# Performance work log

Measured on AMD Instinct MI355X. Metric: run time of the kernel, lower is better.

## Reference

```python
import jax, jax.numpy as jnp
import numpy as np

NUM_HEADS = 16
ROPE_THETA = 10000.0


def _rope_angles(seq_len, head_dim, dtype):
    # lucidrains rotary_embedding_torch: freqs = theta^(-2i/d) for i in 0..d/2,
    # angles = pos * freq, then each angle repeated twice along last dim (interleaved pairs).
    inv_freq = 1.0 / (ROPE_THETA ** (jnp.arange(0, head_dim, 2, dtype=jnp.float32) / head_dim))
    angles = jnp.arange(seq_len, dtype=jnp.float32)[:, None] * inv_freq  # [N, D/2]
    return jnp.repeat(angles, 2, axis=-1).astype(dtype)  # [N, D]


def _rotate_half(t):
    # interleaved pairs: (x0, x1) -> (-x1, x0)
    t1 = t[..., ::2]
    t2 = t[..., 1::2]
    return jnp.stack([-t2, t1], axis=-1).reshape(t.shape)


def _apply_rope(t, cos, sin):
    # t: [B, H, N, D]; cos/sin: [N, D]
    return t * cos + _rotate_half(t) * sin


def setup_inputs() -> dict:
    key = jax.random.key(0)
    ks = jax.random.split(key, 5)
    B, N, C = 4, 1024, 1024
    return {
        "x": jax.random.normal(ks[0], (B, N, C), dtype=jnp.float32),
        "w_qkv": jax.random.normal(ks[1], (C, 3 * C), dtype=jnp.float32) * (C ** -0.5),
        "b_qkv": jax.random.normal(ks[2], (3 * C,), dtype=jnp.float32) * 0.02,
        "w_proj": jax.random.normal(ks[3], (C, C), dtype=jnp.float32) * (C ** -0.5),
        "b_proj": jax.random.normal(ks[4], (C,), dtype=jnp.float32) * 0.02,
    }


def reference(x, w_qkv, b_qkv, w_proj, b_proj):
    B, N, C = x.shape
    H = NUM_HEADS
    D = C // H

    qkv = x @ w_qkv + b_qkv  # [B, N, 3C]
    qkv = qkv.reshape(B, N, 3, H, D).transpose(2, 0, 3, 1, 4)  # [3, B, H, N, D]
    q, k, v = qkv[0], qkv[1], qkv[2]

    ang = _rope_angles(N, D, x.dtype)
    cos, sin = jnp.cos(ang), jnp.sin(ang)
    q = _apply_rope(q, cos, sin)
    k = _apply_rope(k, cos, sin)

    scale = D ** -0.5  # SDPA default scale
    scores = jnp.einsum("bhqd,bhkd->bhqk", q, k) * scale
    attn = jax.nn.softmax(scores, axis=-1)
    out = jnp.einsum("bhqk,bhkd->bhqd", attn, v)  # [B, H, N, D]

    out = out.transpose(0, 2, 1, 3).reshape(B, N, C)
    return out @ w_proj + b_proj
```

## Files before the change

### kernel.cpp

```cpp
#include <hip/hip_runtime.h>
#include <math.h>

#define BB 4
#define NN 1024
#define CC 1024
#define HH 16
#define DD 64
#define N3 3072

typedef __attribute__((ext_vector_type(8))) short bf16x8;
typedef __attribute__((ext_vector_type(8))) _Float16 f16x8;
typedef __attribute__((ext_vector_type(4))) _Float16 f16x4;
typedef __attribute__((ext_vector_type(4))) float f32x4;
typedef __attribute__((ext_vector_type(4))) unsigned int u32x4;

struct ushort4_t { unsigned short x, y, z, w; };

static __device__ __forceinline__ unsigned short f2b(float f) {
    union { float f; unsigned int u; } v; v.f = f;
    unsigned int r = (v.u + 0x7fffu + ((v.u >> 16) & 1u)) >> 16;
    return (unsigned short)r;
}

static __device__ __forceinline__ void ldg_lds16(const void* g, void* l) {
    __builtin_amdgcn_global_load_lds(
        (const __attribute__((address_space(1))) unsigned int*)g,
        (__attribute__((address_space(3))) unsigned int*)l, 16, 0, 0);
}

__global__ __launch_bounds__(256) void prep(const float* __restrict__ x,
                                            const float* __restrict__ wq,
                                            const float* __restrict__ wp,
                                            _Float16* __restrict__ Xh,
                                            _Float16* __restrict__ Wqt,
                                            _Float16* __restrict__ Wpt,
                                            float* __restrict__ ct,
                                            float* __restrict__ st) {
    const int blk = blockIdx.x;
    const int t = threadIdx.x;
    if (blk < 4096) {
        int tid = blk * 256 + t;
        float4 v = ((const float4*)x)[tid];
        f16x4 o = {(_Float16)v.x, (_Float16)v.y, (_Float16)v.z, (_Float16)v.w};
        ((f16x4*)Xh)[tid] = o;
    } else if (blk < 5632) {
        int idx = blk - 4096;
        int n  = (idx % 12) * 256 + t;
        int k0 = (idx / 12) * 8;
        f16x8 o;
        #pragma unroll
        for (int kk = 0; kk < 8; kk++)
            o[kk] = (_Float16)wq[(size_t)(k0 + kk) * N3 + n];
        *(f16x8*)(Wqt + (size_t)n * 1024 + k0) = o;
    } else if (blk < 6144) {
        int idx = blk - 5632;
        int n  = (idx % 4) * 256 + t;
        int k0 = (idx / 4) * 8;
        f16x8 o;
        #pragma unroll
        for (int kk = 0; kk < 8; kk++)
            o[kk] = (_Float16)wp[(size_t)(k0 + kk) * 1024 + n];
        *(f16x8*)(Wpt + (size_t)n * 1024 + k0) = o;
    } else {
        int tid = (blk - 6144) * 256 + t;
        int n = tid >> 5, i = tid & 31;
        double ang = (double)n * exp2(-(double)i * (13.287712379549449 / 32.0));
        ct[tid] = (float)cos(ang);
        st[tid] = (float)sin(ang);
    }
}

static __device__ __forceinline__ void gemm_body_pipe(const char* gA, const char* gB,
                                                      int m0, int n0,
                                                      _Float16* As0, _Float16* As1,
                                                      _Float16* Bs0, _Float16* Bs1,
                                                      int tid, int ln, int qd,
                                                      int wm, int wn, f32x4 acc[4][4]) {
    const int lrow   = tid >> 3;
    const int lchunk = tid & 7;
    const int swz    = (lchunk ^ (lrow & 7)) * 8;

    u32x4 pa[4], pb[4];

    #pragma unroll
    for (int c = 0; c < 4; c++) {
        size_t ra = (size_t)(m0 + c * 32 + lrow) * 2048 + lchunk * 16;
        size_t rb = (size_t)(n0 + c * 32 + lrow) * 2048 + lchunk * 16;
        pa[c] = *(const u32x4*)(gA + ra);
        pb[c] = *(const u32x4*)(gB + rb);
    }
    #pragma unroll
    for (int c = 0; c < 4; c++) {
        *(u32x4*)&As0[(c * 32 + lrow) * 64 + swz] = pa[c];
        *(u32x4*)&Bs0[(c * 32 + lrow) * 64 + swz] = pb[c];
    }
    #pragma unroll
    for (int c = 0; c < 4; c++) {
        size_t ra = (size_t)(m0 + c * 32 + lrow) * 2048 + 128 + lchunk * 16;
        size_t rb = (size_t)(n0 + c * 32 + lrow) * 2048 + 128 + lchunk * 16;
        pa[c] = *(const u32x4*)(gA + ra);
        pb[c] = *(const u32x4*)(gB + rb);
    }
    __syncthreads();

    #pragma unroll
    for (int t = 0; t < 16; t++) {
        const _Float16* Ac = (t & 1) ? As1 : As0;
        const _Float16* Bc = (t & 1) ? Bs1 : Bs0;

        #pragma unroll
        for (int kc = 0; kc < 2; kc++) {
            f16x8 af[4], bf[4];
            #pragma unroll
            for (int i = 0; i < 4; i++)
                af[i] = *(const f16x8*)&Ac[(wm + i * 16 + ln) * 64 +
                                           (((kc * 4 + qd) ^ (ln & 7)) * 8)];
            #pragma unroll
            for (int j = 0; j < 4; j++)
                bf[j] = *(const f16x8*)&Bc[(wn + j * 16 + ln) * 64 +
                                           (((kc * 4 + qd) ^ (ln & 7)) * 8)];
            #pragma unroll
            for (int i = 0; i < 4; i++)
                #pragma unroll
                for (int j = 0; j < 4; j++)
                    acc[i][j] = __builtin_amdgcn_mfma_f32_16x16x32_f16(af[i], bf[j],
                                                                       acc[i][j], 0, 0, 0);
        }

        if (t < 15) {
            _Float16* An = (t & 1) ? As0 : As1;
            _Float16* Bn = (t & 1) ? Bs0 : Bs1;
            #pragma unroll
            for (int c = 0; c < 4; c++) {
                *(u32x4*)&An[(c * 32 + lrow) * 64 + swz] = pa[c];
                *(u32x4*)&Bn[(c * 32 + lrow) * 64 + swz] = pb[c];
            }
            if (t < 14) {
                size_t ko = (size_t)(t + 2) * 128;
                #pragma unroll
                for (int c = 0; c < 4; c++) {
                    size_t ra = (size_t)(m0 + c * 32 + lrow) * 2048 + ko + lchunk * 16;
                    size_t rb = (size_t)(n0 + c * 32 + lrow) * 2048 + ko + lchunk * 16;
                    pa[c] = *(const u32x4*)(gA + ra);
                    pb[c] = *(const u32x4*)(gB + rb);
                }
            }
        }
        __syncthreads();
    }
}

static __device__ __forceinline__ void gemm_body_pipe_n64(const char* gA, const char* gB,
                                                          int m0, int n0,
                                                          _Float16* As0, _Float16* As1,
                                                          _Float16* Bs0, _Float16* Bs1,
                                                          int tid, int ln, int qd,
                                                          int wm, int wn, f32x4 acc[4][2]) {
    const int lrow   = tid >> 3;
    const int lchunk = tid & 7;
    const int swz    = (lchunk ^ (lrow & 7)) * 8;

    u32x4 pa[4], pb[2];

    #pragma unroll
    for (int c = 0; c < 4; c++)
        pa[c] = *(const u32x4*)(gA + (size_t)(m0 + c * 32 + lrow) * 2048 + lchunk * 16);
    #pragma unroll
    for (int c = 0; c < 2; c++)
        pb[c] = *(const u32x4*)(gB + (size_t)(n0 + c * 32 + lrow) * 2048 + lchunk * 16);
    #pragma unroll
    for (int c = 0; c < 4; c++)
        *(u32x4*)&As0[(c * 32 + lrow) * 64 + swz] = pa[c];
    #pragma unroll
    for (int c = 0; c < 2; c++)
        *(u32x4*)&Bs0[(c * 32 + lrow) * 64 + swz] = pb[c];
    #pragma unroll
    for (int c = 0; c < 4; c++)
        pa[c] = *(const u32x4*)(gA + (size_t)(m0 + c * 32 + lrow) * 2048 + 128 + lchunk * 16);
    #pragma unroll
    for (int c = 0; c < 2; c++)
        pb[c] = *(const u32x4*)(gB + (size_t)(n0 + c * 32 + lrow) * 2048 + 128 + lchunk * 16);
    __syncthreads();

    #pragma unroll
    for (int t = 0; t < 16; t++) {
        const _Float16* Ac = (t & 1) ? As1 : As0;
        const _Float16* Bc = (t & 1) ? Bs1 : Bs0;

        #pragma unroll
        for (int kc = 0; kc < 2; kc++) {
            f16x8 af[4], bf[2];
            #pragma unroll
            for (int i = 0; i < 4; i++)
                af[i] = *(const f16x8*)&Ac[(wm + i * 16 + ln) * 64 +
                                           (((kc * 4 + qd) ^ (ln & 7)) * 8)];
            #pragma unroll
            for (int j = 0; j < 2; j++)
                bf[j] = *(const f16x8*)&Bc[(wn + j * 16 + ln) * 64 +
                                           (((kc * 4 + qd) ^ (ln & 7)) * 8)];
            #pragma unroll
            for (int i = 0; i < 4; i++)
                #pragma unroll
                for (int j = 0; j < 2; j++)
                    acc[i][j] = __builtin_amdgcn_mfma_f32_16x16x32_f16(af[i], bf[j],
                                                                       acc[i][j], 0, 0, 0);
        }

        if (t < 15) {
            _Float16* An = (t & 1) ? As0 : As1;
            _Float16* Bn = (t & 1) ? Bs0 : Bs1;
            #pragma unroll
            for (int c = 0; c < 4; c++)
                *(u32x4*)&An[(c * 32 + lrow) * 64 + swz] = pa[c];
            #pragma unroll
            for (int c = 0; c < 2; c++)
                *(u32x4*)&Bn[(c * 32 + lrow) * 64 + swz] = pb[c];
            if (t < 14) {
                size_t ko = (size_t)(t + 2) * 128;
                #pragma unroll
                for (int c = 0; c < 4; c++)
                    pa[c] = *(const u32x4*)(gA + (size_t)(m0 + c * 32 + lrow) * 2048 + ko + lchunk * 16);
                #pragma unroll
                for (int c = 0; c < 2; c++)
                    pb[c] = *(const u32x4*)(gB + (size_t)(n0 + c * 32 + lrow) * 2048 + ko + lchunk * 16);
            }
        }
        __syncthreads();
    }
}

__global__ __launch_bounds__(256) void qkv_mfma(const _Float16* __restrict__ Ah,
                                                const _Float16* __restrict__ Bt,
                                                const float* __restrict__ bias,
                                                const float* __restrict__ cost,
                                                const float* __restrict__ sint,
                                                unsigned short* __restrict__ Q,
                                                unsigned short* __restrict__ K,
                                                unsigned short* __restrict__ Vtg) {
    __shared__ __align__(16) _Float16 As[2][128 * 64];
    __shared__ __align__(16) _Float16 Bs[2][128 * 64];
    const int t = threadIdx.x;
    const int lane = t & 63;
    const int w = t >> 6;
    const int ln = lane & 15, qd = lane >> 4;
    const int n0 = blockIdx.x * 128;
    const int m0 = blockIdx.y * 128;
    const int wm = (w >> 1) * 64, wn = (w & 1) * 64;

    f32x4 acc[4][4];
    #pragma unroll
    for (int i = 0; i < 4; i++)
        #pragma unroll
        for (int j = 0; j < 4; j++) acc[i][j] = (f32x4){0.f, 0.f, 0.f, 0.f};

    gemm_body_pipe((const char*)Ah, (const char*)Bt, m0, n0,
                   As[0], As[1], Bs[0], Bs[1], t, ln, qd, wm, wn, acc);

    const int s = n0 >> 10;
    const int h = ((n0 + wn) >> 6) & 15;
    if (s < 2) {
        unsigned short* dst = (s == 0) ? Q : K;
        const float sc0 = (s == 0) ? 0.125f : 1.0f;
        #pragma unroll
        for (int i = 0; i < 4; i++) {
            #pragma unroll
            for (int reg = 0; reg < 4; reg++) {
                int row = m0 + wm + i * 16 + qd * 4 + reg;
                int b = row >> 10, n = row & 1023;
                size_t obase = (((size_t)(b * HH + h)) * NN + n) * DD;
                #pragma unroll
                for (int j = 0; j < 4; j++) {
                    int d = j * 16 + ln;
                    float v = acc[i][j][reg] + bias[n0 + wn + d];
                    float pv = __shfl_xor(v, 1);
                    float cs = cost[n * 32 + (d >> 1)];
                    float sn = sint[n * 32 + (d >> 1)];
                    float outv = ((d & 1) ? (v * cs + pv * sn) : (v * cs - pv * sn)) * sc0;
                    dst[obase + d] = f2b(outv);
                }
            }
        }
    } else {
        #pragma unroll
        for (int i = 0; i < 4; i++) {
            int row0 = m0 + wm + i * 16 + qd * 4;
            int b = row0 >> 10, n = row0 & 1023;
            size_t tbase = ((size_t)(b * HH + h)) * DD * NN + n;
            #pragma unroll
            for (int j = 0; j < 4; j++) {
                int d = j * 16 + ln;
                float bb = bias[n0 + wn + d];
                ushort4_t pk;
                pk.x = f2b(acc[i][j][0] + bb);
                pk.y = f2b(acc[i][j][1] + bb);
                pk.z = f2b(acc[i][j][2] + bb);
                pk.w = f2b(acc[i][j][3] + bb);
                *(ushort4_t*)&Vtg[tbase + (size_t)d * NN] = pk;
            }
        }
    }
}

__global__ __launch_bounds__(256) void attn_flash(const unsigned short* __restrict__ Qb,
                                                  const unsigned short* __restrict__ Kb,
                                                  const unsigned short* __restrict__ Vtg,
                                                  float* __restrict__ Op,
                                                  float* __restrict__ lp) {
    __shared__ __align__(16) unsigned short Ks[3][64 * 64];
    __shared__ __align__(16) unsigned short Vt[2][64 * 64];
    __shared__ __align__(16) unsigned short Ps[4][16 * 64];

    const int t    = threadIdx.x;
    const int lane = t & 63;
    const int w    = t >> 6;
    const int ln   = lane & 15;
    const int qd   = lane >> 4;
    const int qt   = blockIdx.x >> 1;
    const int kq   = blockIdx.x & 1;
    const int h    = blockIdx.y;
    const int b    = blockIdx.z;
    const size_t base = (size_t)(b * HH + h) * NN * DD;
    const char* Kc = (const char*)(Kb + base);
    const char* Vc = (const char*)(Vtg + base);
    const int xorc = ((lane & 7) ^ (lane >> 3)) * 16;
    const int r8   = lane >> 3;
    const int wrow = w * 16;
    const int kbase = kq * 512;

    bf16x8 qf[2][2];
    #pragma unroll
    for (int g = 0; g < 2; g++) {
        const unsigned short* qp = Qb + base +
            (size_t)(qt * 128 + w * 32 + g * 16 + ln) * DD + qd * 8;
        qf[g][0] = *(const bf16x8*)qp;
        qf[g][1] = *(const bf16x8*)(qp + 32);
    }

    f32x4 o[2][5];
    #pragma unroll
    for (int g = 0; g < 2; g++)
        #pragma unroll
        for (int x = 0; x < 5; x++) o[g][x] = (f32x4){0.f, 0.f, 0.f, 0.f};

    bf16x8 onesf;
    #pragma unroll
    for (int x = 0; x < 8; x++) onesf[x] = (short)0x3F80;

    #pragma unroll
    for (int tile = 0; tile < 3; tile++)
        #pragma unroll
        for (int c = 0; c < 2; c++) {
            int rr = wrow + c * 8 + r8;
            ldg_lds16(Kc + (size_t)(kbase + tile * 64 + rr) * 128 + xorc,
                      &Ks[tile][(wrow + c * 8) * 64]);
        }
    #pragma unroll
    for (int tile = 0; tile < 2; tile++)
        #pragma unroll
        for (int c = 0; c < 2; c++) {
            int rr = wrow + c * 8 + r8;
            ldg_lds16(Vc + (size_t)rr * 2048 + (size_t)(kbase + tile * 64) * 2 + xorc,
                      &Vt[tile][(wrow + c * 8) * 64]);
        }
    __syncthreads();

    f32x4 scur[2][4];
    {
        const unsigned short* KsB = Ks[0];
        #pragma unroll
        for (int j = 0; j < 4; j++) {
            bf16x8 k0f = *(const bf16x8*)&KsB[(ln + 16 * j) * 64 + ((qd ^ (ln & 7)) * 8)];
            bf16x8 k1f = *(const bf16x8*)&KsB[(ln + 16 * j) * 64 + (((4 + qd) ^ (ln & 7)) * 8)];
            #pragma unroll
            for (int g = 0; g < 2; g++) {
                f32x4 sj = {0.f, 0.f, 0.f, 0.f};
                sj = __builtin_amdgcn_mfma_f32_16x16x32_bf16(qf[g][0], k0f, sj, 0, 0, 0);
                sj = __builtin_amdgcn_mfma_f32_16x16x32_bf16(qf[g][1], k1f, sj, 0, 0, 0);
                scur[g][j] = sj;
            }
        }
    }

    const float C1 = 1.44269504f;
    const float C0 = -16.0f * 1.44269504f;

    #pragma unroll
    for (int tt = 0; tt < 8; tt++) {
        f32x4 snext[2][4];
        if (tt < 7) {
            const unsigned short* KsB = Ks[(tt + 1) % 3];
            #pragma unroll
            for (int j = 0; j < 4; j++) {
                bf16x8 k0f = *(const bf16x8*)&KsB[(ln + 16 * j) * 64 + ((qd ^ (ln & 7)) * 8)];
                bf16x8 k1f = *(const bf16x8*)&KsB[(ln + 16 * j) * 64 + (((4 + qd) ^ (ln & 7)) * 8)];
                #pragma unroll
                for (int g = 0; g < 2; g++) {
                    f32x4 sj = {0.f, 0.f, 0.f, 0.f};
                    sj = __builtin_amdgcn_mfma_f32_16x16x32_bf16(qf[g][0], k0f, sj, 0, 0, 0);
                    sj = __builtin_amdgcn_mfma_f32_16x16x32_bf16(qf[g][1], k1f, sj, 0, 0, 0);
                    snext[g][j] = sj;
                }
            }
        }

        {
            const unsigned short* VtB = Vt[tt & 1];
            bf16x8 v0f[4], v1f[4];
            #pragma unroll
            for (int j = 0; j < 4; j++) {
                v0f[j] = *(const bf16x8*)&VtB[(ln + 16 * j) * 64 + ((qd ^ (ln & 7)) * 8)];
                v1f[j] = *(const bf16x8*)&VtB[(ln + 16 * j) * 64 + (((4 + qd) ^ (ln & 7)) * 8)];
            }
            unsigned short* PsB = &Ps[w][0];
            #pragma unroll
            for (int g = 0; g < 2; g++) {
                #pragma unroll
                for (int j = 0; j < 4; j++)
                    #pragma unroll
                    for (int r = 0; r < 4; r++) {
                        float p = exp2f(fmaf(scur[g][j][r], C1, C0));
                        union { float f; unsigned int u; } cv; cv.f = p;
                        int m = qd * 4 + r;
                        PsB[m * 64 + ((((ln >> 3) + 2 * j) ^ (m & 7)) * 8) + (ln & 7)] =
                            (unsigned short)((cv.u + 0x8000u) >> 16);
                    }
                bf16x8 pf0 = *(const bf16x8*)&PsB[ln * 64 + ((qd ^ (ln & 7)) * 8)];
                bf16x8 pf1 = *(const bf16x8*)&PsB[ln * 64 + (((4 + qd) ^ (ln & 7)) * 8)];
                #pragma unroll
                for (int j = 0; j < 4; j++) {
                    o[g][j] = __builtin_amdgcn_mfma_f32_16x16x32_bf16(pf0, v0f[j], o[g][j], 0, 0, 0);
                    o[g][j] = __builtin_amdgcn_mfma_f32_16x16x32_bf16(pf1, v1f[j], o[g][j], 0, 0, 0);
                }
                o[g][4] = __builtin_amdgcn_mfma_f32_16x16x32_bf16(pf0, onesf, o[g][4], 0, 0, 0);
                o[g][4] = __builtin_amdgcn_mfma_f32_16x16x32_bf16(pf1, onesf, o[g][4], 0, 0, 0);
            }
        }

        __syncthreads();

        if (tt <= 4) {
            int tile = tt + 3;
            #pragma unroll
            for (int c = 0; c < 2; c++) {
                int rr = wrow + c * 8 + r8;
                ldg_lds16(Kc + (size_t)(kbase + tile * 64 + rr) * 128 + xorc,
                          &Ks[tt % 3][(wrow + c * 8) * 64]);
            }
        }
        if (tt <= 5) {
            int tile = tt + 2;
            #pragma unroll
            for (int c = 0; c < 2; c++) {
                int rr = wrow + c * 8 + r8;
                ldg_lds16(Vc + (size_t)rr * 2048 + (size_t)(kbase + tile * 64) * 2 + xorc,
                          &Vt[tt & 1][(wrow + c * 8) * 64]);
            }
        }

        #pragma unroll
        for (int g = 0; g < 2; g++)
            #pragma unroll
            for (int j = 0; j < 4; j++) scur[g][j] = snext[g][j];
    }

    #pragma unroll
    for (int g = 0; g < 2; g++)
        #pragma unroll
        for (int r = 0; r < 4; r++) {
            int q = qt * 128 + w * 32 + g * 16 + qd * 4 + r;
            size_t rb = (((size_t)b * NN + q) * HH + h) * DD;
            float* op = Op + (size_t)kq * 4194304 + rb + ln;
            op[0]  = o[g][0][r];
            op[16] = o[g][1][r];
            op[32] = o[g][2][r];
            op[48] = o[g][3][r];
            if (ln == 0)
                lp[kq * 65536 + (((size_t)b * NN + q) * HH + h)] = o[g][4][r];
        }
}

__global__ __launch_bounds__(256) void merge_kernel(const float* __restrict__ O1,
                                                    const float* __restrict__ O2,
                                                    const float* __restrict__ l1,
                                                    const float* __restrict__ l2,
                                                    _Float16* __restrict__ AO) {
    int i = blockIdx.x * 256 + threadIdx.x;
    float4 a = ((const float4*)O1)[i];
    float4 c = ((const float4*)O2)[i];
    int row = i >> 4;
    float inv = 1.0f / (l1[row] + l2[row]);
    f16x4 o = {(_Float16)((a.x + c.x) * inv), (_Float16)((a.y + c.y) * inv),
               (_Float16)((a.z + c.z) * inv), (_Float16)((a.w + c.w) * inv)};
    ((f16x4*)AO)[i] = o;
}

__global__ __launch_bounds__(256) void proj_mfma(const _Float16* __restrict__ Ah,
                                                 const _Float16* __restrict__ Bt,
                                                 const float* __restrict__ bias,
                                                 float* __restrict__ out) {
    __shared__ __align__(16) _Float16 As[2][128 * 64];
    __shared__ __align__(16) _Float16 Bs[2][64 * 64];
    const int t = threadIdx.x;
    const int lane = t & 63;
    const int w = t >> 6;
    const int ln = lane & 15, qd = lane >> 4;
    const int n0 = blockIdx.x * 64;
    const int m0 = blockIdx.y * 128;
    const int wm = (w >> 1) * 64, wn = (w & 1) * 32;

    f32x4 acc[4][2];
    #pragma unroll
    for (int i = 0; i < 4; i++)
        #pragma unroll
        for (int j = 0; j < 2; j++) acc[i][j] = (f32x4){0.f, 0.f, 0.f, 0.f};

    gemm_body_pipe_n64((const char*)Ah, (const char*)Bt, m0, n0,
                       As[0], As[1], Bs[0], Bs[1], t, ln, qd, wm, wn, acc);

    #pragma unroll
    for (int i = 0; i < 4; i++) {
        #pragma unroll
        for (int reg = 0; reg < 4; reg++) {
            int row = m0 + wm + i * 16 + qd * 4 + reg;
            #pragma unroll
            for (int j = 0; j < 2; j++) {
                int col = n0 + wn + j * 16 + ln;
                out[(size_t)row * 1024 + col] = acc[i][j][reg] + bias[col];
            }
        }
    }
}

extern "C" void kernel_launch(void* const* d_in, const int* in_sizes, int n_in,
                              void* d_out, int out_size, void* d_ws, size_t ws_size,
                              hipStream_t stream) {
    const float* x      = (const float*)d_in[0];
    const float* w_qkv  = (const float*)d_in[1];
    const float* b_qkv  = (const float*)d_in[2];
    const float* w_proj = (const float*)d_in[3];
    const float* b_proj = (const float*)d_in[4];
    float* out = (float*)d_out;

    char* ws = (char*)d_ws;
    _Float16* Xh   = (_Float16*)(ws);
    _Float16* Wqt  = (_Float16*)(ws + (8u << 20));
    _Float16* Wpt  = (_Float16*)(ws + (14u << 20));
    unsigned short* Q  = (unsigned short*)(ws + (16u << 20));
    unsigned short* K  = (unsigned short*)(ws + (24u << 20));
    unsigned short* Vt = (unsigned short*)(ws + (32u << 20));
    _Float16* AOh  = (_Float16*)(ws + (40u << 20));
    float* cost    = (float*)(ws + (48u << 20));
    float* sint    = (float*)(ws + (48u << 20) + (128u << 10));
    float* Opf     = (float*)(ws + (56u << 20));
    float* lpf     = (float*)(ws + (88u << 20));

    prep<<<6272, 256, 0, stream>>>(x, w_qkv, w_proj, Xh, Wqt, Wpt, cost, sint);
    qkv_mfma<<<dim3(24, 32), 256, 0, stream>>>(Xh, Wqt, b_qkv, cost, sint, Q, K, Vt);
    attn_flash<<<dim3(16, 16, 4), 256, 0, stream>>>(Q, K, Vt, Opf, lpf);
    merge_kernel<<<4096, 256, 0, stream>>>(Opf, Opf + 4194304, lpf, lpf + 65536, AOh);
    proj_mfma<<<dim3(16, 32), 256, 0, stream>>>(AOh, Wpt, b_proj, out);
}
```

Before: 186.6 us.

## Store split-K attention partials in fp16 and double-buffer K tiles

Attention partial outputs are now written as fp16 instead of fp32, which halves the traffic for the partial-output write and for the merge kernel's read. The K shared-memory buffer goes from triple to double buffering and is loaded together with V, with an extra barrier after each refill. Shared memory use drops, which may allow more resident blocks, but the extra barrier serializes loads against compute. Unnormalized partial sums stored in fp16 could lose precision or overflow.

Result: no change. 185.6 us (-0.6%).

```diff
diff --git a/kernel.cpp b/kernel.cpp
--- a/kernel.cpp
+++ b/kernel.cpp
@@ -304,9 +304,9 @@
 __global__ __launch_bounds__(256) void attn_flash(const unsigned short* __restrict__ Qb,
                                                   const unsigned short* __restrict__ Kb,
                                                   const unsigned short* __restrict__ Vtg,
-                                                  float* __restrict__ Op,
+                                                  _Float16* __restrict__ Op,
                                                   float* __restrict__ lp) {
-    __shared__ __align__(16) unsigned short Ks[3][64 * 64];
+    __shared__ __align__(16) unsigned short Ks[2][64 * 64];
     __shared__ __align__(16) unsigned short Vt[2][64 * 64];
     __shared__ __align__(16) unsigned short Ps[4][16 * 64];
 
@@ -347,18 +347,12 @@
     for (int x = 0; x < 8; x++) onesf[x] = (short)0x3F80;
 
     #pragma unroll
-    for (int tile = 0; tile < 3; tile++)
+    for (int tile = 0; tile < 2; tile++)
         #pragma unroll
         for (int c = 0; c < 2; c++) {
             int rr = wrow + c * 8 + r8;
             ldg_lds16(Kc + (size_t)(kbase + tile * 64 + rr) * 128 + xorc,
                       &Ks[tile][(wrow + c * 8) * 64]);
-        }
-    #pragma unroll
-    for (int tile = 0; tile < 2; tile++)
-        #pragma unroll
-        for (int c = 0; c < 2; c++) {
-            int rr = wrow + c * 8 + r8;
             ldg_lds16(Vc + (size_t)rr * 2048 + (size_t)(kbase + tile * 64) * 2 + xorc,
                       &Vt[tile][(wrow + c * 8) * 64]);
         }
@@ -388,7 +382,7 @@
     for (int tt = 0; tt < 8; tt++) {
         f32x4 snext[2][4];
         if (tt < 7) {
-            const unsigned short* KsB = Ks[(tt + 1) % 3];
+            const unsigned short* KsB = Ks[(tt + 1) & 1];
             #pragma unroll
             for (int j = 0; j < 4; j++) {
                 bf16x8 k0f = *(const bf16x8*)&KsB[(ln + 16 * j) * 64 + ((qd ^ (ln & 7)) * 8)];
@@ -438,23 +432,17 @@
 
         __syncthreads();
 
-        if (tt <= 4) {
-            int tile = tt + 3;
+        if (tt < 6) {
+            int tile = tt + 2;
             #pragma unroll
             for (int c = 0; c < 2; c++) {
                 int rr = wrow + c * 8 + r8;
                 ldg_lds16(Kc + (size_t)(kbase + tile * 64 + rr) * 128 + xorc,
-                          &Ks[tt % 3][(wrow + c * 8) * 64]);
-            }
-        }
-        if (tt <= 5) {
-            int tile = tt + 2;
-            #pragma unroll
-            for (int c = 0; c < 2; c++) {
-                int rr = wrow + c * 8 + r8;
+                          &Ks[tt & 1][(wrow + c * 8) * 64]);
                 ldg_lds16(Vc + (size_t)rr * 2048 + (size_t)(kbase + tile * 64) * 2 + xorc,
                           &Vt[tt & 1][(wrow + c * 8) * 64]);
             }
+            __syncthreads();
         }
 
         #pragma unroll
@@ -469,28 +457,30 @@
         for (int r = 0; r < 4; r++) {
             int q = qt * 128 + w * 32 + g * 16 + qd * 4 + r;
             size_t rb = (((size_t)b * NN + q) * HH + h) * DD;
-            float* op = Op + (size_t)kq * 4194304 + rb + ln;
-            op[0]  = o[g][0][r];
-            op[16] = o[g][1][r];
-            op[32] = o[g][2][r];
-            op[48] = o[g][3][r];
+            _Float16* op = Op + (size_t)kq * 4194304 + rb + ln;
+            op[0]  = (_Float16)o[g][0][r];
+            op[16] = (_Float16)o[g][1][r];
+            op[32] = (_Float16)o[g][2][r];
+            op[48] = (_Float16)o[g][3][r];
             if (ln == 0)
                 lp[kq * 65536 + (((size_t)b * NN + q) * HH + h)] = o[g][4][r];
         }
 }
 
-__global__ __launch_bounds__(256) void merge_kernel(const float* __restrict__ O1,
-                                                    const float* __restrict__ O2,
+__global__ __launch_bounds__(256) void merge_kernel(const _Float16* __restrict__ O1,
+                                                    const _Float16* __restrict__ O2,
                                                     const float* __restrict__ l1,
                                                     const float* __restrict__ l2,
                                                     _Float16* __restrict__ AO) {
     int i = blockIdx.x * 256 + threadIdx.x;
-    float4 a = ((const float4*)O1)[i];
-    float4 c = ((const float4*)O2)[i];
+    f16x4 a = ((const f16x4*)O1)[i];
+    f16x4 c = ((const f16x4*)O2)[i];
     int row = i >> 4;
     float inv = 1.0f / (l1[row] + l2[row]);
-    f16x4 o = {(_Float16)((a.x + c.x) * inv), (_Float16)((a.y + c.y) * inv),
-               (_Float16)((a.z + c.z) * inv), (_Float16)((a.w + c.w) * inv)};
+    f16x4 o = {(_Float16)(((float)a[0] + (float)c[0]) * inv),
+               (_Float16)(((float)a[1] + (float)c[1]) * inv),
+               (_Float16)(((float)a[2] + (float)c[2]) * inv),
+               (_Float16)(((float)a[3] + (float)c[3]) * inv)};
     ((f16x4*)AO)[i] = o;
 }
 
@@ -551,8 +541,8 @@
     _Float16* AOh  = (_Float16*)(ws + (40u << 20));
     float* cost    = (float*)(ws + (48u << 20));
     float* sint    = (float*)(ws + (48u << 20) + (128u << 10));
-    float* Opf     = (float*)(ws + (56u << 20));
-    float* lpf     = (float*)(ws + (88u << 20));
+    _Float16* Opf  = (_Float16*)(ws + (56u << 20));
+    float* lpf     = (float*)(ws + (72u << 20));
 
     prep<<<6272, 256, 0, stream>>>(x, w_qkv, w_proj, Xh, Wqt, Wpt, cost, sint);
     qkv_mfma<<<dim3(24, 32), 256, 0, stream>>>(Xh, Wqt, b_qkv, cost, sint, Q, K, Vt);
```
